# Kernel tuning notes

Measured on AMD Instinct MI355X. Metric: run time of the kernel, lower is better.

Reference implementation:

```python
import jax, jax.numpy as jnp
import numpy as np

COMMITMENT_COST = 0.25
EPS_NORM = 1e-12  # F.normalize eps
EPS_LOG = 1e-10


def _l2norm(x):
    # F.normalize(x, dim=-1): x / max(||x||, eps)
    n = jnp.linalg.norm(x, axis=-1, keepdims=True)
    return x / jnp.maximum(n, EPS_NORM)


def setup_inputs() -> dict:
    key = jax.random.key(0)
    k1, k2 = jax.random.split(key)
    f_emb = jax.random.normal(k1, (16, 8192, 256), dtype=jnp.float32)
    W = jax.random.normal(k2, (1024, 256), dtype=jnp.float32)  # embedding.weight, N(0,1) init
    return {"f_emb": f_emb, "W": W}


def reference(f_emb, W):
    K, D = W.shape
    flat = f_emb.reshape(-1, D)                       # [N, D]
    fn = _l2norm(flat)                                # normalized inputs
    en = _l2norm(W)                                   # normalized codebook
    # squared L2 distances between normalized vectors: [N, K]
    distances = (jnp.sum(fn * fn, axis=1, keepdims=True)
                 + jnp.sum(en * en, axis=1)
                 - 2.0 * jnp.matmul(fn, en.T))
    encoding_indices = jnp.argmin(distances, axis=1)  # [N]
    encodings = jax.nn.one_hot(encoding_indices, K, dtype=f_emb.dtype)  # [N, K]
    # one-hot @ W == gather; same math, no dense matmul needed
    quantized = W[encoding_indices].reshape(f_emb.shape)
    qn = _l2norm(quantized)
    xn = _l2norm(f_emb)
    e_latent_loss = jnp.mean((jax.lax.stop_gradient(qn) - xn) ** 2)
    q_latent_loss = jnp.mean((qn - jax.lax.stop_gradient(xn)) ** 2)
    latent_loss = q_latent_loss + COMMITMENT_COST * e_latent_loss
    # straight-through estimator
    quantized_st = xn + jax.lax.stop_gradient(qn - xn)
    avg_probs = jnp.mean(encodings, axis=0)
    perplexity = jnp.exp(-jnp.sum(avg_probs * jnp.log(avg_probs + EPS_LOG)))
    return quantized_st, latent_loss, perplexity, encodings
```

## Files before the change

### kernel.cpp

```cpp
#include <hip/hip_runtime.h>
#include <hip/hip_bf16.h>
#include <stdint.h>

#define NROWS 131072
#define KCODES 1024
#define DDIM 256
#define BM 128
#define BN 128
#define BK 32

typedef __attribute__((ext_vector_type(4))) float f32x4;
typedef __attribute__((ext_vector_type(8))) short s16x8;
typedef __attribute__((ext_vector_type(4))) short s16x4;

__device__ __forceinline__ unsigned short f2bf(float f) {
  unsigned int u = __float_as_uint(f);
  u += 0x7FFFu + ((u >> 16) & 1u);
  return (unsigned short)(u >> 16);
}
__device__ __forceinline__ float bf2f(unsigned short h) {
  return __uint_as_float(((unsigned int)h) << 16);
}
__device__ __forceinline__ float wred(float v) {
#pragma unroll
  for (int s = 1; s < 64; s <<= 1) v += __shfl_xor(v, s, 64);
  return v;
}

__global__ __launch_bounds__(256) void prep_w(const float* __restrict__ W,
    float* __restrict__ en, unsigned short* __restrict__ enh,
    unsigned short* __restrict__ enl, float* __restrict__ ensq) {
  int wid = threadIdx.x >> 6, lane = threadIdx.x & 63;
  int k = blockIdx.x * 4 + wid;
  float4 w4 = ((const float4*)(W + (size_t)k * DDIM))[lane];
  float ss = wred(w4.x * w4.x + w4.y * w4.y + w4.z * w4.z + w4.w * w4.w);
  float mx = fmaxf(sqrtf(ss), 1e-12f);
  float4 e4;
  e4.x = w4.x / mx; e4.y = w4.y / mx; e4.z = w4.z / mx; e4.w = w4.w / mx;
  ((float4*)(en + (size_t)k * DDIM))[lane] = e4;
  unsigned short h0 = f2bf(e4.x), h1 = f2bf(e4.y), h2 = f2bf(e4.z), h3 = f2bf(e4.w);
  s16x4 hv = { (short)h0, (short)h1, (short)h2, (short)h3 };
  s16x4 lv = { (short)f2bf(e4.x - bf2f(h0)), (short)f2bf(e4.y - bf2f(h1)),
               (short)f2bf(e4.z - bf2f(h2)), (short)f2bf(e4.w - bf2f(h3)) };
  ((s16x4*)(enh + (size_t)k * DDIM))[lane] = hv;
  ((s16x4*)(enl + (size_t)k * DDIM))[lane] = lv;
  float sq = wred(e4.x * e4.x + e4.y * e4.y + e4.z * e4.z + e4.w * e4.w);
  if (lane == 0) ensq[k] = sq;
}

__global__ __launch_bounds__(256) void prep_f(const float* __restrict__ f,
    unsigned short* __restrict__ fnh, unsigned short* __restrict__ fnl) {
  int wid = threadIdx.x >> 6, lane = threadIdx.x & 63;
  int n = blockIdx.x * 4 + wid;
  float4 v = ((const float4*)(f + (size_t)n * DDIM))[lane];
  float ss = wred(v.x * v.x + v.y * v.y + v.z * v.z + v.w * v.w);
  float mx = fmaxf(sqrtf(ss), 1e-12f);
  float4 e4;
  e4.x = v.x / mx; e4.y = v.y / mx; e4.z = v.z / mx; e4.w = v.w / mx;
  unsigned short h0 = f2bf(e4.x), h1 = f2bf(e4.y), h2 = f2bf(e4.z), h3 = f2bf(e4.w);
  s16x4 hv = { (short)h0, (short)h1, (short)h2, (short)h3 };
  s16x4 lv = { (short)f2bf(e4.x - bf2f(h0)), (short)f2bf(e4.y - bf2f(h1)),
               (short)f2bf(e4.z - bf2f(h2)), (short)f2bf(e4.w - bf2f(h3)) };
  ((s16x4*)(fnh + (size_t)n * DDIM))[lane] = hv;
  ((s16x4*)(fnl + (size_t)n * DDIM))[lane] = lv;
}

__global__ __launch_bounds__(256, 2) void gemm3(
    const unsigned short* __restrict__ fnh, const unsigned short* __restrict__ fnl,
    const unsigned short* __restrict__ enh, const unsigned short* __restrict__ enl,
    const float* __restrict__ ensq, float2* __restrict__ partials) {
  __shared__ unsigned short lds[2][4][BM * BK];
  int t = threadIdx.x;
  int bid = blockIdx.x;
  int x = bid & 7, jj = bid >> 3;
  int rt = x * 128 + (jj >> 3);
  int ct = jj & 7;
  int bm0 = rt * BM, bc0 = ct * BN;
  int lane = t & 63, wid = t >> 6;
  int wr = wid >> 1, wc = wid & 1;
  int l15 = lane & 15, h4 = lane >> 4;

  f32x4 acc[4][4] = {};

  const unsigned short* bases[4] = { fnh, fnl, enh, enl };

  auto stage = [&](int buf, int kt) {
#pragma unroll
    for (int q = 0; q < 4; ++q) {
      const unsigned short* bp = bases[q];
      int rbase = (q < 2) ? bm0 : bc0;
#pragma unroll
      for (int i = 0; i < 2; ++i) {
        int ci = i * 256 + t;
        int row = ci >> 2;
        int kc = (((ci & 3) ^ (row & 3)) << 3);
        const void* src = bp + (size_t)(rbase + row) * DDIM + kt * BK + kc;
        void* dst = (void*)&lds[buf][q][(i * 256 + wid * 64) * 8];
        __builtin_amdgcn_global_load_lds(
            (const __attribute__((address_space(1))) unsigned int*)src,
            (__attribute__((address_space(3))) unsigned int*)dst, 16, 0, 0);
      }
    }
  };

  stage(0, 0);
  for (int kt = 0; kt < 8; ++kt) {
    __syncthreads();
    if (kt < 7) stage((kt + 1) & 1, kt + 1);
    int buf = kt & 1;
    s16x8 ah[4], al[4], bh[4], bl[4];
#pragma unroll
    for (int m = 0; m < 4; ++m) {
      int row = wr * 64 + m * 16 + l15;
      int ro = row * BK + ((h4 ^ (row & 3)) << 3);
      ah[m] = *(const s16x8*)&lds[buf][0][ro];
      al[m] = *(const s16x8*)&lds[buf][1][ro];
    }
#pragma unroll
    for (int n = 0; n < 4; ++n) {
      int row = wc * 64 + n * 16 + l15;
      int ro = row * BK + ((h4 ^ (row & 3)) << 3);
      bh[n] = *(const s16x8*)&lds[buf][2][ro];
      bl[n] = *(const s16x8*)&lds[buf][3][ro];
    }
#pragma unroll
    for (int m = 0; m < 4; ++m)
#pragma unroll
      for (int n = 0; n < 4; ++n) {
        acc[m][n] = __builtin_amdgcn_mfma_f32_16x16x32_bf16(ah[m], bh[n], acc[m][n], 0, 0, 0);
        acc[m][n] = __builtin_amdgcn_mfma_f32_16x16x32_bf16(ah[m], bl[n], acc[m][n], 0, 0, 0);
        acc[m][n] = __builtin_amdgcn_mfma_f32_16x16x32_bf16(al[m], bh[n], acc[m][n], 0, 0, 0);
      }
  }

  float esq[4];
#pragma unroll
  for (int n = 0; n < 4; ++n) esq[n] = ensq[bc0 + wc * 64 + n * 16 + l15];

  float2* red = (float2*)lds;
#pragma unroll
  for (int m = 0; m < 4; ++m) {
#pragma unroll
    for (int j = 0; j < 4; ++j) {
      float bd = fmaf(-2.f, acc[m][0][j], esq[0]);
      int bc_ = bc0 + wc * 64 + l15;
#pragma unroll
      for (int n = 1; n < 4; ++n) {
        float d = fmaf(-2.f, acc[m][n][j], esq[n]);
        int c = bc0 + wc * 64 + n * 16 + l15;
        if (d < bd) { bd = d; bc_ = c; }
      }
#pragma unroll
      for (int s = 1; s < 16; s <<= 1) {
        float od = __shfl_xor(bd, s, 64);
        int oc = __shfl_xor(bc_, s, 64);
        if (od < bd || (od == bd && oc < bc_)) { bd = od; bc_ = oc; }
      }
      if (l15 == 0)
        red[wc * BM + wr * 64 + m * 16 + h4 * 4 + j] = make_float2(bd, __int_as_float(bc_));
    }
  }
  __syncthreads();
  if (t < BM) {
    float2 p0 = red[t];
    float2 p1 = red[BM + t];
    float d = p0.x; int c = __float_as_int(p0.y);
    int c1 = __float_as_int(p1.y);
    if (p1.x < d || (p1.x == d && c1 < c)) { d = p1.x; c = c1; }
    partials[(size_t)(bm0 + t) * 8 + ct] = make_float2(d, __int_as_float(c));
  }
}

__global__ __launch_bounds__(256) void reduce_k(const float2* __restrict__ partials,
                                                int* __restrict__ idx) {
  int r = blockIdx.x * 256 + threadIdx.x;
  const float2* p = partials + (size_t)r * 8;
  float d = p[0].x; int c = __float_as_int(p[0].y);
#pragma unroll
  for (int i = 1; i < 8; ++i) {
    float2 q = p[i];
    int qc = __float_as_int(q.y);
    if (q.x < d || (q.x == d && qc < c)) { d = q.x; c = qc; }
  }
  idx[r] = c;
}

__global__ __launch_bounds__(256) void outputs_k(const float* __restrict__ f,
    const int* __restrict__ idx, const float* __restrict__ en,
    float* __restrict__ outq, float* __restrict__ enc,
    int* __restrict__ hist, double* __restrict__ lacc) {
  int wid = threadIdx.x >> 6, lane = threadIdx.x & 63;
  int n = blockIdx.x * 4 + wid;
  int id = idx[n];
  float4 fv = ((const float4*)(f + (size_t)n * DDIM))[lane];
  float ss = wred(fv.x * fv.x + fv.y * fv.y + fv.z * fv.z + fv.w * fv.w);
  float mx = fmaxf(sqrtf(ss), 1e-12f);
  float4 ev = ((const float4*)(en + (size_t)id * DDIM))[lane];
  ((float4*)(outq + (size_t)n * DDIM))[lane] = ev;
  float dx = ev.x - fv.x / mx;
  float dy = ev.y - fv.y / mx;
  float dz = ev.z - fv.z / mx;
  float dw = ev.w - fv.w / mx;
  float ls = wred(dx * dx + dy * dy + dz * dz + dw * dw);
  if (lane == 0) {
    atomicAdd(&lacc[blockIdx.x & 255], (double)ls);
    atomicAdd(&hist[id], 1);
  }
  float* rowp = enc + (size_t)n * KCODES + lane * 16;
#pragma unroll
  for (int i = 0; i < 8; ++i) {
    int c0 = lane * 16 + i * 2;
    ((float2*)rowp)[i] = make_float2(c0 == id ? 1.f : 0.f, (c0 + 1) == id ? 1.f : 0.f);
  }
}

__global__ __launch_bounds__(256) void finalize_k(const int* __restrict__ hist,
    const double* __restrict__ lacc, float* __restrict__ out) {
  __shared__ double sd[256];
  __shared__ double se[256];
  int t = threadIdx.x;
  double e = 0.0;
#pragma unroll
  for (int i = 0; i < 4; ++i) {
    int c = hist[t * 4 + i];
    float p = (float)c * (1.0f / 131072.0f);
    e += (double)(p * logf(p + 1e-10f));
  }
  sd[t] = lacc[t];
  se[t] = e;
  __syncthreads();
  for (int s = 128; s > 0; s >>= 1) {
    if (t < s) { sd[t] += sd[t + s]; se[t] += se[t + s]; }
    __syncthreads();
  }
  if (t == 0) {
    out[33554432] = (float)(1.25 * (sd[0] / ((double)NROWS * (double)DDIM)));
    out[33554433] = expf(-(float)se[0]);
  }
}

extern "C" void kernel_launch(void* const* d_in, const int* in_sizes, int n_in,
                              void* d_out, int out_size, void* d_ws, size_t ws_size,
                              hipStream_t stream) {
  const float* f = (const float*)d_in[0];
  const float* W = (const float*)d_in[1];
  float* out = (float*)d_out;
  char* ws = (char*)d_ws;

  int*    hist = (int*)ws;
  double* lacc = (double*)(ws + 4096);
  float*  ensq = (float*)(ws + 8192);
  float*  en   = (float*)(ws + 12288);
  unsigned short* enh = (unsigned short*)(ws + 12288 + 1048576);
  unsigned short* enl = (unsigned short*)(ws + 12288 + 1048576 + 524288);
  int*    idx  = (int*)(ws + 12288 + 2097152);

  char* ob = (char*)d_out;
  const size_t S = 134217984;
  unsigned short* fnh = (unsigned short*)(ob + S);
  unsigned short* fnl = (unsigned short*)(ob + S + 67108864);
  float2* partials = (float2*)(ob + S + 134217728);
  float* enc = out + 33554434;

  hipMemsetAsync(ws, 0, 8192, stream);
  prep_w<<<KCODES / 4, 256, 0, stream>>>(W, en, enh, enl, ensq);
  prep_f<<<NROWS / 4, 256, 0, stream>>>(f, fnh, fnl);
  gemm3<<<(NROWS / BM) * (KCODES / BN), 256, 0, stream>>>(fnh, fnl, enh, enl, ensq, partials);
  reduce_k<<<NROWS / 256, 256, 0, stream>>>(partials, idx);
  outputs_k<<<NROWS / 4, 256, 0, stream>>>(f, idx, en, out, enc, hist, lacc);
  finalize_k<<<1, 256, 0, stream>>>(hist, lacc, out);
}
```

Baseline: 1.148 ms.

## Fuse full-codebook argmin into GEMM blocks and write one-hot by memset plus scatter

```diff
diff --git a/kernel.cpp b/kernel.cpp
--- a/kernel.cpp
+++ b/kernel.cpp
@@ -6,7 +6,6 @@
 #define KCODES 1024
 #define DDIM 256
 #define BM 128
-#define BN 128
 #define BK 32
 
 typedef __attribute__((ext_vector_type(4))) float f32x4;
@@ -68,58 +67,67 @@
 __global__ __launch_bounds__(256, 2) void gemm3(
     const unsigned short* __restrict__ fnh, const unsigned short* __restrict__ fnl,
     const unsigned short* __restrict__ enh, const unsigned short* __restrict__ enl,
-    const float* __restrict__ ensq, float2* __restrict__ partials) {
+    const float* __restrict__ ensq, int* __restrict__ idx) {
   __shared__ unsigned short lds[2][4][BM * BK];
   int t = threadIdx.x;
-  int bid = blockIdx.x;
-  int x = bid & 7, jj = bid >> 3;
-  int rt = x * 128 + (jj >> 3);
-  int ct = jj & 7;
-  int bm0 = rt * BM, bc0 = ct * BN;
+  int bm0 = blockIdx.x * BM;
   int lane = t & 63, wid = t >> 6;
   int wr = wid >> 1, wc = wid & 1;
   int l15 = lane & 15, h4 = lane >> 4;
 
+  float run_d[4][4];
+  int run_c[4][4];
+#pragma unroll
+  for (int m = 0; m < 4; ++m)
+#pragma unroll
+    for (int j = 0; j < 4; ++j) { run_d[m][j] = 1e30f; run_c[m][j] = 0; }
+
+  auto stage = [&](int buf, int it) {
+    int ct = it >> 3, kt = it & 7;
+#pragma unroll
+    for (int i = 0; i < 2; ++i) {
+      int ci = i * 256 + t;
+      int row = ci >> 2;
+      int kc = (((ci & 3) ^ ((row >> 2) & 3)) << 3);
+      int koff = kt * BK + kc;
+      unsigned int dstb = (unsigned int)((i * 256 + wid * 64) * 8);
+      const unsigned short* sAh = fnh + (size_t)(bm0 + row) * DDIM + koff;
+      const unsigned short* sAl = fnl + (size_t)(bm0 + row) * DDIM + koff;
+      const unsigned short* sBh = enh + (size_t)(ct * 128 + row) * DDIM + koff;
+      const unsigned short* sBl = enl + (size_t)(ct * 128 + row) * DDIM + koff;
+      __builtin_amdgcn_global_load_lds(
+          (const __attribute__((address_space(1))) unsigned int*)sAh,
+          (__attribute__((address_space(3))) unsigned int*)&lds[buf][0][dstb], 16, 0, 0);
+      __builtin_amdgcn_global_load_lds(
+          (const __attribute__((address_space(1))) unsigned int*)sAl,
+          (__attribute__((address_space(3))) unsigned int*)&lds[buf][1][dstb], 16, 0, 0);
+      __builtin_amdgcn_global_load_lds(
+          (const __attribute__((address_space(1))) unsigned int*)sBh,
+          (__attribute__((address_space(3))) unsigned int*)&lds[buf][2][dstb], 16, 0, 0);
+      __builtin_amdgcn_global_load_lds(
+          (const __attribute__((address_space(1))) unsigned int*)sBl,
+          (__attribute__((address_space(3))) unsigned int*)&lds[buf][3][dstb], 16, 0, 0);
+    }
+  };
+
   f32x4 acc[4][4] = {};
-
-  const unsigned short* bases[4] = { fnh, fnl, enh, enl };
-
-  auto stage = [&](int buf, int kt) {
-#pragma unroll
-    for (int q = 0; q < 4; ++q) {
-      const unsigned short* bp = bases[q];
-      int rbase = (q < 2) ? bm0 : bc0;
-#pragma unroll
-      for (int i = 0; i < 2; ++i) {
-        int ci = i * 256 + t;
-        int row = ci >> 2;
-        int kc = (((ci & 3) ^ (row & 3)) << 3);
-        const void* src = bp + (size_t)(rbase + row) * DDIM + kt * BK + kc;
-        void* dst = (void*)&lds[buf][q][(i * 256 + wid * 64) * 8];
-        __builtin_amdgcn_global_load_lds(
-            (const __attribute__((address_space(1))) unsigned int*)src,
-            (__attribute__((address_space(3))) unsigned int*)dst, 16, 0, 0);
-      }
-    }
-  };
-
   stage(0, 0);
-  for (int kt = 0; kt < 8; ++kt) {
+  for (int it = 0; it < 64; ++it) {
     __syncthreads();
-    if (kt < 7) stage((kt + 1) & 1, kt + 1);
-    int buf = kt & 1;
+    if (it < 63) stage((it + 1) & 1, it + 1);
+    int buf = it & 1;
     s16x8 ah[4], al[4], bh[4], bl[4];
 #pragma unroll
     for (int m = 0; m < 4; ++m) {
       int row = wr * 64 + m * 16 + l15;
-      int ro = row * BK + ((h4 ^ (row & 3)) << 3);
+      int ro = row * BK + ((h4 ^ ((row >> 2) & 3)) << 3);
       ah[m] = *(const s16x8*)&lds[buf][0][ro];
       al[m] = *(const s16x8*)&lds[buf][1][ro];
     }
 #pragma unroll
     for (int n = 0; n < 4; ++n) {
       int row = wc * 64 + n * 16 + l15;
-      int ro = row * BK + ((h4 ^ (row & 3)) << 3);
+      int ro = row * BK + ((h4 ^ ((row >> 2) & 3)) << 3);
       bh[n] = *(const s16x8*)&lds[buf][2][ro];
       bl[n] = *(const s16x8*)&lds[buf][3][ro];
     }
@@ -131,58 +139,48 @@
         acc[m][n] = __builtin_amdgcn_mfma_f32_16x16x32_bf16(ah[m], bl[n], acc[m][n], 0, 0, 0);
         acc[m][n] = __builtin_amdgcn_mfma_f32_16x16x32_bf16(al[m], bh[n], acc[m][n], 0, 0, 0);
       }
-  }
-
-  float esq[4];
-#pragma unroll
-  for (int n = 0; n < 4; ++n) esq[n] = ensq[bc0 + wc * 64 + n * 16 + l15];
+    if ((it & 7) == 7) {
+      int ct = it >> 3;
+#pragma unroll
+      for (int n = 0; n < 4; ++n) {
+        float es = ensq[ct * 128 + wc * 64 + n * 16 + l15];
+        int c = ct * 128 + wc * 64 + n * 16 + l15;
+#pragma unroll
+        for (int m = 0; m < 4; ++m)
+#pragma unroll
+          for (int j = 0; j < 4; ++j) {
+            float d = fmaf(-2.f, acc[m][n][j], es);
+            if (d < run_d[m][j]) { run_d[m][j] = d; run_c[m][j] = c; }
+            acc[m][n][j] = 0.f;
+          }
+      }
+    }
+  }
 
   float2* red = (float2*)lds;
 #pragma unroll
-  for (int m = 0; m < 4; ++m) {
+  for (int m = 0; m < 4; ++m)
 #pragma unroll
     for (int j = 0; j < 4; ++j) {
-      float bd = fmaf(-2.f, acc[m][0][j], esq[0]);
-      int bc_ = bc0 + wc * 64 + l15;
-#pragma unroll
-      for (int n = 1; n < 4; ++n) {
-        float d = fmaf(-2.f, acc[m][n][j], esq[n]);
-        int c = bc0 + wc * 64 + n * 16 + l15;
-        if (d < bd) { bd = d; bc_ = c; }
-      }
+      float bd = run_d[m][j];
+      int bc = run_c[m][j];
 #pragma unroll
       for (int s = 1; s < 16; s <<= 1) {
         float od = __shfl_xor(bd, s, 64);
-        int oc = __shfl_xor(bc_, s, 64);
-        if (od < bd || (od == bd && oc < bc_)) { bd = od; bc_ = oc; }
+        int oc = __shfl_xor(bc, s, 64);
+        if (od < bd || (od == bd && oc < bc)) { bd = od; bc = oc; }
       }
       if (l15 == 0)
-        red[wc * BM + wr * 64 + m * 16 + h4 * 4 + j] = make_float2(bd, __int_as_float(bc_));
-    }
-  }
+        red[wc * BM + wr * 64 + m * 16 + h4 * 4 + j] = make_float2(bd, __int_as_float(bc));
+    }
   __syncthreads();
   if (t < BM) {
     float2 p0 = red[t];
     float2 p1 = red[BM + t];
-    float d = p0.x; int c = __float_as_int(p0.y);
-    int c1 = __float_as_int(p1.y);
-    if (p1.x < d || (p1.x == d && c1 < c)) { d = p1.x; c = c1; }
-    partials[(size_t)(bm0 + t) * 8 + ct] = make_float2(d, __int_as_float(c));
-  }
-}
-
-__global__ __launch_bounds__(256) void reduce_k(const float2* __restrict__ partials,
-                                                int* __restrict__ idx) {
-  int r = blockIdx.x * 256 + threadIdx.x;
-  const float2* p = partials + (size_t)r * 8;
-  float d = p[0].x; int c = __float_as_int(p[0].y);
-#pragma unroll
-  for (int i = 1; i < 8; ++i) {
-    float2 q = p[i];
-    int qc = __float_as_int(q.y);
-    if (q.x < d || (q.x == d && qc < c)) { d = q.x; c = qc; }
-  }
-  idx[r] = c;
+    int c0 = __float_as_int(p0.y), c1 = __float_as_int(p1.y);
+    int c = (p1.x < p0.x || (p1.x == p0.x && c1 < c0)) ? c1 : c0;
+    idx[bm0 + t] = c;
+  }
 }
 
 __global__ __launch_bounds__(256) void outputs_k(const float* __restrict__ f,
@@ -205,12 +203,7 @@
   if (lane == 0) {
     atomicAdd(&lacc[blockIdx.x & 255], (double)ls);
     atomicAdd(&hist[id], 1);
-  }
-  float* rowp = enc + (size_t)n * KCODES + lane * 16;
-#pragma unroll
-  for (int i = 0; i < 8; ++i) {
-    int c0 = lane * 16 + i * 2;
-    ((float2*)rowp)[i] = make_float2(c0 == id ? 1.f : 0.f, (c0 + 1) == id ? 1.f : 0.f);
+    enc[(size_t)n * KCODES + id] = 1.0f;
   }
 }
 
@@ -259,14 +252,13 @@
   const size_t S = 134217984;
   unsigned short* fnh = (unsigned short*)(ob + S);
   unsigned short* fnl = (unsigned short*)(ob + S + 67108864);
-  float2* partials = (float2*)(ob + S + 134217728);
   float* enc = out + 33554434;
 
   hipMemsetAsync(ws, 0, 8192, stream);
   prep_w<<<KCODES / 4, 256, 0, stream>>>(W, en, enh, enl, ensq);
   prep_f<<<NROWS / 4, 256, 0, stream>>>(f, fnh, fnl);
-  gemm3<<<(NROWS / BM) * (KCODES / BN), 256, 0, stream>>>(fnh, fnl, enh, enl, ensq, partials);
-  reduce_k<<<NROWS / 256, 256, 0, stream>>>(partials, idx);
+  gemm3<<<NROWS / BM, 256, 0, stream>>>(fnh, fnl, enh, enl, ensq, idx);
+  hipMemsetAsync((void*)enc, 0, 536870912ULL, stream);
   outputs_k<<<NROWS / 4, 256, 0, stream>>>(f, idx, en, out, enc, hist, lacc);
   finalize_k<<<1, 256, 0, stream>>>(hist, lacc, out);
 }
```

Result: faster. 1.042 ms (-9.2%).
